# Kernel tuning notes

Hardware: AMD Instinct MI355X
Metric: run time of the kernel (lower is better)

The kernel has to match this reference:

```python
import jax, jax.numpy as jnp
import numpy as np

B, S, D = 2, 512, 256

def setup_inputs() -> dict:
    key = jax.random.key(0)
    k1, k2, k3, k4, k5 = jax.random.split(key, 5)
    return {
        "query": jax.random.normal(k1, (B, S, D), dtype=jnp.float32),
        "key": jax.random.normal(k2, (B, S, D), dtype=jnp.float32),
        "value": jax.random.normal(k3, (B, S, D), dtype=jnp.float32),
        "Wm_w": jax.random.normal(k4, (D, D), dtype=jnp.float32) * (1.0 / np.sqrt(D)),
        "vm_w": jax.random.normal(k5, (1, D), dtype=jnp.float32) * (1.0 / np.sqrt(D)),
    }

def reference(query, key, value, Wm_w, vm_w):
    # pairwise difference: q.unsqueeze(1) - q.unsqueeze(2) -> [B, S, S, D]
    diff = query[:, None, :, :] - query[:, :, None, :]
    # Wm (Linear, no bias): [B,S,S,D] @ Wm_w^T, then tanh
    h = jnp.tanh(jnp.einsum('bijd,ed->bije', diff, Wm_w))
    # vm (Linear D->1, no bias) + squeeze -> scores [B, S, S]
    sjt = jnp.einsum('bije,e->bij', h, vm_w[0])
    # softmax over dim=2 (eval mode: dropout is identity)
    atten = jax.nn.softmax(sjt, axis=2)
    # bmm(atten, value) -> [B, S, D]
    context = jnp.einsum('bij,bjd->bid', atten, value)
    return context, atten
```

## Files before the change

### kernel.cpp

```cpp
#include <hip/hip_runtime.h>

#define B 2
#define S 512
#define D 256
#define C2L 2.885390081777927f
#define LOG2E 1.4426950408889634f

__global__ __launch_bounds__(256) void proj_kernel(const float* __restrict__ q,
                                                   const float* __restrict__ W,
                                                   float* __restrict__ EJ,
                                                   float* __restrict__ EN) {
    __shared__ float qlds[4 * D];
    const int t = threadIdx.x;
    const int b = blockIdx.x / (S / 4);
    const int i0 = (blockIdx.x % (S / 4)) * 4;
    const float* qbase = q + (size_t)(b * S + i0) * D;
    for (int idx = t; idx < 4 * D; idx += 256) qlds[idx] = qbase[idx];
    __syncthreads();
    const float* wr = W + (size_t)t * D;
    float a0 = 0.f, a1 = 0.f, a2 = 0.f, a3 = 0.f;
#pragma unroll 4
    for (int d = 0; d < D; ++d) {
        float w = wr[d];
        a0 = fmaf(qlds[d], w, a0);
        a1 = fmaf(qlds[D + d], w, a1);
        a2 = fmaf(qlds[2 * D + d], w, a2);
        a3 = fmaf(qlds[3 * D + d], w, a3);
    }
    a0 *= C2L; a1 *= C2L; a2 *= C2L; a3 *= C2L;
    float* ej = EJ + (size_t)(b * D + t) * S + i0;
    *(float4*)ej = make_float4(__builtin_amdgcn_exp2f(a0), __builtin_amdgcn_exp2f(a1),
                               __builtin_amdgcn_exp2f(a2), __builtin_amdgcn_exp2f(a3));
    EN[(size_t)(b * S + i0 + 0) * D + t] = __builtin_amdgcn_exp2f(-a0);
    EN[(size_t)(b * S + i0 + 1) * D + t] = __builtin_amdgcn_exp2f(-a1);
    EN[(size_t)(b * S + i0 + 2) * D + t] = __builtin_amdgcn_exp2f(-a2);
    EN[(size_t)(b * S + i0 + 3) * D + t] = __builtin_amdgcn_exp2f(-a3);
}

__global__ __launch_bounds__(512) void fused_kernel(const float* __restrict__ EJ,
                                                    const float* __restrict__ EN,
                                                    const float* __restrict__ vm,
                                                    const float* __restrict__ value,
                                                    float* __restrict__ att,
                                                    float* __restrict__ ctx) {
    __shared__ float en4[D][4];
    __shared__ float wl[D];
    __shared__ float a4[S][4];
    __shared__ float part[4][8][64][4];
    __shared__ float redm[4][8], reds[4][8];

    const int t = threadIdx.x;
    const int b = blockIdx.x >> 7;
    const int i0 = (blockIdx.x & 127) * 4;

    if (t < D) wl[t] = -2.f * vm[t];
    {
        const int e = t & 255, r2 = (t >> 8) * 2;
        en4[e][r2]     = EN[((size_t)(b * S + i0 + r2)) * D + e];
        en4[e][r2 + 1] = EN[((size_t)(b * S + i0 + r2 + 1)) * D + e];
    }
    __syncthreads();

    float acc[4] = {};
    const float* ejp = EJ + (size_t)b * D * S + t;
#pragma unroll 8
    for (int e = 0; e < D; ++e) {
        float ev = ejp[(size_t)e * S];
        float w = wl[e];
        float4 f = *(const float4*)&en4[e][0];
        float y0 = fmaf(ev, f.x, 1.f);
        float y1 = fmaf(ev, f.y, 1.f);
        float y2 = fmaf(ev, f.z, 1.f);
        float y3 = fmaf(ev, f.w, 1.f);
        float r0 = __builtin_amdgcn_rcpf(y0);
        float r2v = __builtin_amdgcn_rcpf(y2);
        float r1 = __uint_as_float(0x7EF311C3u - __float_as_uint(y1));
        r1 = r1 * fmaf(-y1, r1, 2.f);
        r1 = r1 * fmaf(-y1, r1, 2.f);
        float r3 = __uint_as_float(0x7EF311C3u - __float_as_uint(y3));
        r3 = r3 * fmaf(-y3, r3, 2.f);
        r3 = r3 * fmaf(-y3, r3, 2.f);
        acc[0] = fmaf(w, r0, acc[0]);
        acc[1] = fmaf(w, r1, acc[1]);
        acc[2] = fmaf(w, r2v, acc[2]);
        acc[3] = fmaf(w, r3, acc[3]);
    }

    const int lane = t & 63, wv = t >> 6;
#pragma unroll
    for (int r = 0; r < 4; ++r) {
        float lm = acc[r];
#pragma unroll
        for (int off = 32; off; off >>= 1) lm = fmaxf(lm, __shfl_xor(lm, off));
        if (lane == 0) redm[r][wv] = lm;
    }
    __syncthreads();
    float p[4];
#pragma unroll
    for (int r = 0; r < 4; ++r) {
        float m = redm[r][0];
#pragma unroll
        for (int w = 1; w < 8; ++w) m = fmaxf(m, redm[r][w]);
        p[r] = __builtin_amdgcn_exp2f((acc[r] - m) * LOG2E);
        float ls = p[r];
#pragma unroll
        for (int off = 32; off; off >>= 1) ls += __shfl_xor(ls, off);
        if (lane == 0) reds[r][wv] = ls;
    }
    __syncthreads();
#pragma unroll
    for (int r = 0; r < 4; ++r) {
        float s = 0.f;
#pragma unroll
        for (int w = 0; w < 8; ++w) s += reds[r][w];
        float a = p[r] * __builtin_amdgcn_rcpf(s);
        a4[t][r] = a;
        att[(size_t)(b * S + i0 + r) * S + t] = a;
    }
    __syncthreads();

    {
        const int dq = t & 63, js = t >> 6;
        float4 acc0 = {}, acc1 = {}, acc2 = {}, acc3 = {};
        const float* vb = value + (size_t)b * S * D + (size_t)dq * 4;
#pragma unroll 4
        for (int jj = 0; jj < 64; ++jj) {
            int j = js * 64 + jj;
            float4 v = *(const float4*)(vb + (size_t)j * D);
            float w0 = a4[j][0], w1 = a4[j][1], w2 = a4[j][2], w3 = a4[j][3];
            acc0.x = fmaf(w0, v.x, acc0.x); acc0.y = fmaf(w0, v.y, acc0.y);
            acc0.z = fmaf(w0, v.z, acc0.z); acc0.w = fmaf(w0, v.w, acc0.w);
            acc1.x = fmaf(w1, v.x, acc1.x); acc1.y = fmaf(w1, v.y, acc1.y);
            acc1.z = fmaf(w1, v.z, acc1.z); acc1.w = fmaf(w1, v.w, acc1.w);
            acc2.x = fmaf(w2, v.x, acc2.x); acc2.y = fmaf(w2, v.y, acc2.y);
            acc2.z = fmaf(w2, v.z, acc2.z); acc2.w = fmaf(w2, v.w, acc2.w);
            acc3.x = fmaf(w3, v.x, acc3.x); acc3.y = fmaf(w3, v.y, acc3.y);
            acc3.z = fmaf(w3, v.z, acc3.z); acc3.w = fmaf(w3, v.w, acc3.w);
        }
        *(float4*)&part[0][js][dq][0] = acc0;
        *(float4*)&part[1][js][dq][0] = acc1;
        *(float4*)&part[2][js][dq][0] = acc2;
        *(float4*)&part[3][js][dq][0] = acc3;
    }
    __syncthreads();
    if (t < 256) {
        const int row = t >> 6, dq = t & 63;
        float4 sum = {};
#pragma unroll
        for (int js = 0; js < 8; ++js) {
            float4 pt = *(const float4*)&part[row][js][dq][0];
            sum.x += pt.x; sum.y += pt.y; sum.z += pt.z; sum.w += pt.w;
        }
        *(float4*)(ctx + (size_t)(b * S + i0 + row) * D + (size_t)dq * 4) = sum;
    }
}

extern "C" void kernel_launch(void* const* d_in, const int* in_sizes, int n_in,
                              void* d_out, int out_size, void* d_ws, size_t ws_size,
                              hipStream_t stream) {
    const float* q = (const float*)d_in[0];
    const float* value = (const float*)d_in[2];
    const float* W = (const float*)d_in[3];
    const float* vm = (const float*)d_in[4];

    float* ctx = (float*)d_out;
    float* att = ctx + (size_t)B * S * D;
    float* EJ = (float*)d_ws;
    float* EN = EJ + (size_t)B * D * S;

    proj_kernel<<<B * (S / 4), 256, 0, stream>>>(q, W, EJ, EN);
    fused_kernel<<<B * (S / 4), 512, 0, stream>>>(EJ, EN, vm, value, att, ctx);
}
```

Before: 48.43 us.

## Interleave EJ in groups of four and use packed f32x2 math in score loop

The projection kernel now writes EJ in an interleaved layout where four consecutive e-values for each column sit together. The fused kernel can then load them with one float4 per thread instead of four scalar strided loads. The inner score loop is rewritten with 2-wide float vectors, aiming for packed FMA/sub instructions on CDNA for the y computation, the Newton reciprocal and the accumulation. The EN staging is also reordered so the row pairs match the packed layout. The cost is scattered scalar stores in the projection kernel and more complex indexing.

After: 44.57 us. 1.09x faster.

```diff
diff --git a/kernel.cpp b/kernel.cpp
--- a/kernel.cpp
+++ b/kernel.cpp
@@ -6,9 +6,12 @@
 #define C2L 2.885390081777927f
 #define LOG2E 1.4426950408889634f
 
+typedef float f32x2 __attribute__((ext_vector_type(2)));
+typedef unsigned int u32x2 __attribute__((ext_vector_type(2)));
+
 __global__ __launch_bounds__(256) void proj_kernel(const float* __restrict__ q,
                                                    const float* __restrict__ W,
-                                                   float* __restrict__ EJ,
+                                                   float* __restrict__ EJ4,
                                                    float* __restrict__ EN) {
     __shared__ float qlds[4 * D];
     const int t = threadIdx.x;
@@ -28,16 +31,18 @@
         a3 = fmaf(qlds[3 * D + d], w, a3);
     }
     a0 *= C2L; a1 *= C2L; a2 *= C2L; a3 *= C2L;
-    float* ej = EJ + (size_t)(b * D + t) * S + i0;
-    *(float4*)ej = make_float4(__builtin_amdgcn_exp2f(a0), __builtin_amdgcn_exp2f(a1),
-                               __builtin_amdgcn_exp2f(a2), __builtin_amdgcn_exp2f(a3));
+    float* ejb = EJ4 + (((size_t)(b * 64 + (t >> 2))) * S + i0) * 4 + (t & 3);
+    ejb[0]  = __builtin_amdgcn_exp2f(a0);
+    ejb[4]  = __builtin_amdgcn_exp2f(a1);
+    ejb[8]  = __builtin_amdgcn_exp2f(a2);
+    ejb[12] = __builtin_amdgcn_exp2f(a3);
     EN[(size_t)(b * S + i0 + 0) * D + t] = __builtin_amdgcn_exp2f(-a0);
     EN[(size_t)(b * S + i0 + 1) * D + t] = __builtin_amdgcn_exp2f(-a1);
     EN[(size_t)(b * S + i0 + 2) * D + t] = __builtin_amdgcn_exp2f(-a2);
     EN[(size_t)(b * S + i0 + 3) * D + t] = __builtin_amdgcn_exp2f(-a3);
 }
 
-__global__ __launch_bounds__(512) void fused_kernel(const float* __restrict__ EJ,
+__global__ __launch_bounds__(512) void fused_kernel(const float* __restrict__ EJ4,
                                                     const float* __restrict__ EN,
                                                     const float* __restrict__ vm,
                                                     const float* __restrict__ value,
@@ -55,41 +60,48 @@
 
     if (t < D) wl[t] = -2.f * vm[t];
     {
-        const int e = t & 255, r2 = (t >> 8) * 2;
-        en4[e][r2]     = EN[((size_t)(b * S + i0 + r2)) * D + e];
-        en4[e][r2 + 1] = EN[((size_t)(b * S + i0 + r2 + 1)) * D + e];
+        const int e = t & 255, rsel = t >> 8;
+        float v0 = EN[((size_t)(b * S + i0 + rsel)) * D + e];
+        float v2 = EN[((size_t)(b * S + i0 + rsel + 2)) * D + e];
+        en4[e][rsel * 2 + 0] = v0;
+        en4[e][rsel * 2 + 1] = v2;
     }
     __syncthreads();
 
-    float acc[4] = {};
-    const float* ejp = EJ + (size_t)b * D * S + t;
-#pragma unroll 8
-    for (int e = 0; e < D; ++e) {
-        float ev = ejp[(size_t)e * S];
-        float w = wl[e];
-        float4 f = *(const float4*)&en4[e][0];
-        float y0 = fmaf(ev, f.x, 1.f);
-        float y1 = fmaf(ev, f.y, 1.f);
-        float y2 = fmaf(ev, f.z, 1.f);
-        float y3 = fmaf(ev, f.w, 1.f);
-        float r0 = __builtin_amdgcn_rcpf(y0);
-        float r2v = __builtin_amdgcn_rcpf(y2);
-        float r1 = __uint_as_float(0x7EF311C3u - __float_as_uint(y1));
-        r1 = r1 * fmaf(-y1, r1, 2.f);
-        r1 = r1 * fmaf(-y1, r1, 2.f);
-        float r3 = __uint_as_float(0x7EF311C3u - __float_as_uint(y3));
-        r3 = r3 * fmaf(-y3, r3, 2.f);
-        r3 = r3 * fmaf(-y3, r3, 2.f);
-        acc[0] = fmaf(w, r0, acc[0]);
-        acc[1] = fmaf(w, r1, acc[1]);
-        acc[2] = fmaf(w, r2v, acc[2]);
-        acc[3] = fmaf(w, r3, acc[3]);
+    f32x2 acc02 = {0.f, 0.f}, acc13 = {0.f, 0.f};
+    const float4* ejp = (const float4*)EJ4 + (size_t)b * 64 * S + t;
+    const f32x2 one2 = {1.f, 1.f}, two2 = {2.f, 2.f};
+    const u32x2 magic = {0x7EF311C3u, 0x7EF311C3u};
+#pragma unroll 4
+    for (int g = 0; g < 64; ++g) {
+        float4 ev4 = ejp[(size_t)g * S];
+#pragma unroll
+        for (int c = 0; c < 4; ++c) {
+            const float ev = (c == 0) ? ev4.x : (c == 1) ? ev4.y : (c == 2) ? ev4.z : ev4.w;
+            const int e = g * 4 + c;
+            float4 f = *(const float4*)&en4[e][0];
+            const float w = wl[e];
+            f32x2 ev2 = {ev, ev};
+            f32x2 f02 = {f.x, f.y}, f13 = {f.z, f.w};
+            f32x2 y02 = ev2 * f02 + one2;
+            f32x2 y13 = ev2 * f13 + one2;
+            f32x2 r02 = {__builtin_amdgcn_rcpf(y02.x),
+                         __builtin_amdgcn_rcpf(y02.y)};
+            u32x2 ui = magic - __builtin_bit_cast(u32x2, y13);
+            f32x2 rn = __builtin_bit_cast(f32x2, ui);
+            rn = rn * (two2 - y13 * rn);
+            rn = rn * (two2 - y13 * rn);
+            f32x2 w2 = {w, w};
+            acc02 += w2 * r02;
+            acc13 += w2 * rn;
+        }
     }
+    float accR[4] = {acc02.x, acc13.x, acc02.y, acc13.y};
 
     const int lane = t & 63, wv = t >> 6;
 #pragma unroll
     for (int r = 0; r < 4; ++r) {
-        float lm = acc[r];
+        float lm = accR[r];
 #pragma unroll
         for (int off = 32; off; off >>= 1) lm = fmaxf(lm, __shfl_xor(lm, off));
         if (lane == 0) redm[r][wv] = lm;
@@ -101,7 +113,7 @@
         float m = redm[r][0];
 #pragma unroll
         for (int w = 1; w < 8; ++w) m = fmaxf(m, redm[r][w]);
-        p[r] = __builtin_amdgcn_exp2f((acc[r] - m) * LOG2E);
+        p[r] = __builtin_amdgcn_exp2f((accR[r] - m) * LOG2E);
         float ls = p[r];
 #pragma unroll
         for (int off = 32; off; off >>= 1) ls += __shfl_xor(ls, off);
@@ -165,9 +177,9 @@
 
     float* ctx = (float*)d_out;
     float* att = ctx + (size_t)B * S * D;
-    float* EJ = (float*)d_ws;
-    float* EN = EJ + (size_t)B * D * S;
+    float* EJ4 = (float*)d_ws;
+    float* EN = EJ4 + (size_t)B * D * S;
 
-    proj_kernel<<<B * (S / 4), 256, 0, stream>>>(q, W, EJ, EN);
-    fused_kernel<<<B * (S / 4), 512, 0, stream>>>(EJ, EN, vm, value, att, ctx);
+    proj_kernel<<<B * (S / 4), 256, 0, stream>>>(q, W, EJ4, EN);
+    fused_kernel<<<B * (S / 4), 512, 0, stream>>>(EJ4, EN, vm, value, att, ctx);
 }
```
